# Kernel tuning notes

Hardware: AMD Instinct MI355X
Metric: run time of the kernel (lower is better)

Reference implementation:

```python
import jax, jax.numpy as jnp
import numpy as np

B, T, I, U = 64, 1024, 512, 1024


def ternary_quantize(w):
    # alpha = mean|w|; threshold = 0.7*alpha; map to {-alpha, 0, alpha}
    alpha = jnp.mean(jnp.abs(w))
    thr = 0.7 * alpha
    w_t = jnp.where(jnp.abs(w) < thr, jnp.zeros_like(w), jnp.sign(w))
    return alpha * w_t


def setup_inputs() -> dict:
    key = jax.random.key(0)
    k1, k2, k3 = jax.random.split(key, 3)
    x = jax.random.normal(k1, (B, T, I), dtype=jnp.float32)
    kernel = jax.random.normal(k2, (I, 4 * U), dtype=jnp.float32) * 0.05
    recurrent_kernel = jax.random.normal(k3, (U, 4 * U), dtype=jnp.float32) * 0.05
    # keras unit_forget_bias: zeros except ones on the forget-gate quarter
    bias = jnp.concatenate([jnp.zeros((U,)), jnp.ones((U,)), jnp.zeros((2 * U,))]).astype(jnp.float32)
    return {"x": x, "kernel": kernel, "recurrent_kernel": recurrent_kernel, "bias": bias}


def reference(x, kernel, recurrent_kernel, bias):
    kq = ternary_quantize(kernel)            # [I, 4U]
    rq = ternary_quantize(recurrent_kernel)  # [U, 4U]
    # Precompute input projection for all timesteps (math identical to per-step matmul)
    xz = jnp.einsum('bti,ig->btg', x, kq) + bias  # [B, T, 4U]
    xz_t = jnp.transpose(xz, (1, 0, 2))           # [T, B, 4U]

    def step(carry, zx):
        h, c = carry
        z = zx + h @ rq                            # [B, 4U]
        zi, zf, zg, zo = jnp.split(z, 4, axis=-1)  # keras gate order i, f, c, o
        i = jax.nn.sigmoid(zi)
        f = jax.nn.sigmoid(zf)
        g = jnp.tanh(zg)
        o = jax.nn.sigmoid(zo)
        c_new = f * c + i * g
        h_new = o * jnp.tanh(c_new)
        return (h_new, c_new), h_new

    h0 = jnp.zeros((x.shape[0], U), dtype=x.dtype)
    c0 = jnp.zeros((x.shape[0], U), dtype=x.dtype)
    _, hs = jax.lax.scan(step, (h0, c0), xz_t)     # hs: [T, B, U]
    return jnp.transpose(hs, (1, 0, 2))            # return_sequences=True -> [B, T, U]
```

## Files before the change

### kernel.cpp

```cpp
#include <hip/hip_runtime.h>
#include <hip/hip_bf16.h>


typedef __attribute__((ext_vector_type(8))) __bf16 bf16x8;
typedef __attribute__((ext_vector_type(4))) float f32x4;

#define NWG 256
#define WGT 512
#define T_N 1024

__global__ void absum_kernel(const float* __restrict__ w, int n,
                             double* __restrict__ partial) {
  __shared__ double sd[256];
  double s = 0.0;
  for (int i = blockIdx.x * 256 + threadIdx.x; i < n; i += 256 * 256)
    s += fabs((double)w[i]);
  sd[threadIdx.x] = s;
  __syncthreads();
  for (int k = 128; k > 0; k >>= 1) {
    if (threadIdx.x < k) sd[threadIdx.x] += sd[threadIdx.x + k];
    __syncthreads();
  }
  if (threadIdx.x == 0) partial[blockIdx.x] = sd[0];
}

__global__ void alpha_finalize(const double* __restrict__ pk,
                               const double* __restrict__ pr,
                               float* __restrict__ alphas) {
  __shared__ double sd[256];
  int t = threadIdx.x;
  sd[t] = pk[t];
  __syncthreads();
  for (int s = 128; s > 0; s >>= 1) {
    if (t < s) sd[t] += sd[t + s];
    __syncthreads();
  }
  if (t == 0) alphas[0] = (float)(sd[0] / (512.0 * 4096.0));
  __syncthreads();
  sd[t] = pr[t];
  __syncthreads();
  for (int s = 128; s > 0; s >>= 1) {
    if (t < s) sd[t] += sd[t + s];
    __syncthreads();
  }
  if (t == 0) alphas[1] = (float)(sd[0] / (1024.0 * 4096.0));
}

__global__ void quant_kernel(const float* __restrict__ w, int kbits,
                             const float* __restrict__ alphas, int ai,
                             __hip_bfloat16* __restrict__ wt, int total) {
  int idx = blockIdx.x * 256 + threadIdx.x;
  if (idx >= total) return;
  float thr = 0.7f * alphas[ai];
  int K = 1 << kbits;
  int c = idx >> kbits;
  int k = idx & (K - 1);
  float v = w[k * 4096 + (c & 3) * 1024 + (c >> 2)];
  float q = (fabsf(v) < thr) ? 0.0f : ((v > 0.0f) ? 1.0f : ((v < 0.0f) ? -1.0f : 0.0f));
  wt[idx] = __float2bfloat16(q);
}

__device__ __forceinline__ bf16x8 cvt2(f32x4 a, f32x4 b) {
  bf16x8 r;
  r[0] = (__bf16)a[0]; r[1] = (__bf16)a[1];
  r[2] = (__bf16)a[2]; r[3] = (__bf16)a[3];
  r[4] = (__bf16)b[0]; r[5] = (__bf16)b[1];
  r[6] = (__bf16)b[2]; r[7] = (__bf16)b[3];
  return r;
}
__device__ __forceinline__ void ld_cc16(bf16x8* d, const __hip_bfloat16* p) {
  asm volatile("global_load_dwordx4 %0, %1, off sc0 sc1"
               : "=v"(*d) : "v"(p) : "memory");
}
__device__ __forceinline__ void st_cc2(__hip_bfloat16* p, unsigned bits) {
  asm volatile("global_store_short %0, %1, off sc0 sc1" ::"v"(p), "v"(bits)
               : "memory");
}
__device__ __forceinline__ unsigned bf16b(float f) {
  return (unsigned)__builtin_bit_cast(unsigned short, __float2bfloat16(f));
}
__device__ __forceinline__ float sigm(float z) { return 1.0f / (1.0f + __expf(-z)); }
__device__ __forceinline__ float tanhx(float z) {
  float e = __expf(-2.0f * fabsf(z));
  return __builtin_copysignf((1.0f - e) / (1.0f + e), z);
}
__device__ __forceinline__ void wg_barrier_wait(const int* gctr, int g, int tgt,
                                                int* lflag, int epoch,
                                                int lane, int wave) {
  if (wave == 0) {
    const int* p = gctr + (g * 4 + (lane & 3)) * 32;
    for (;;) {
      int v = (lane < 4) ? __hip_atomic_load(p, __ATOMIC_RELAXED,
                                             __HIP_MEMORY_SCOPE_AGENT)
                         : tgt;
      if (__all(v >= tgt)) break;
      __builtin_amdgcn_s_sleep(1);
    }
    if (lane == 0)
      __hip_atomic_store(lflag, epoch, __ATOMIC_RELEASE,
                         __HIP_MEMORY_SCOPE_WORKGROUP);
  }
  while (__hip_atomic_load(lflag, __ATOMIC_ACQUIRE,
                           __HIP_MEMORY_SCOPE_WORKGROUP) < epoch) {}
}

__global__ void __launch_bounds__(WGT, 2)
lstm_persist(const float* __restrict__ bias4, const float* __restrict__ alphas,
             const float* __restrict__ x,
             const __hip_bfloat16* __restrict__ wtk,
             const __hip_bfloat16* __restrict__ wtr,
             __hip_bfloat16* __restrict__ hbuf,
             float* __restrict__ out,
             int* __restrict__ gctr) {
  extern __shared__ char lds[];
  char* lwr = lds;
  float* lz = (float*)(lds + 131072);
  float* lxz = (float*)(lds + 148480);
  int* lflag = (int*)(lds + 157184);

  const int tid = threadIdx.x;
  const int wg = blockIdx.x;
  const int g = wg >> 6;
  const int u = wg & 63;
  const int rb0 = g << 4;
  const int lane = tid & 63;
  const int wave = tid >> 6;
  const int r16 = lane & 15;
  const int kb8 = (lane >> 4) << 3;

  if (tid == 0) *lflag = 0;

  for (int it = tid; it < 8192; it += WGT) {
    int c = it >> 7, kk = (it & 127) << 3;
    bf16x8 v = *(const bf16x8*)(wtr + (size_t)(u * 64 + c) * 1024 + kk);
    *(bf16x8*)(lwr + (c << 11) + ((kk * 2) ^ ((c & 7) << 4))) = v;
  }

  const float ak = alphas[0];
  const float ar = alphas[1];

  const int rl = (tid >> 4) & 15;
  const int ul = tid & 15;
  float bias_c[4];
#pragma unroll
  for (int gg = 0; gg < 4; ++gg)
    bias_c[gg] = bias4[gg * 1024 + u * 16 + ul];
  float cst = 0.0f;
  __hip_bfloat16* hst = hbuf + ((rb0 + rl) << 10) + u * 16 + ul;
  float* outp = out + ((size_t)(rb0 + rl) << 20) + u * 16 + ul;

  const int ks0 = wave << 8;
  float* lzw = lz + wave * 1088;

  const int cw = wave - 4;

  bf16x8 fr[8];

  auto xproj = [&](int tt, int par) {
    const float* xr = x + ((size_t)(rb0 + r16) << 19) + ((size_t)tt << 9) + kb8;
    const __hip_bfloat16* bp =
        wtk + (size_t)(u * 64 + cw * 16 + r16) * 512 + kb8;
    f32x4 a = {0.f, 0.f, 0.f, 0.f};
#pragma unroll
    for (int kw = 0; kw < 16; ++kw) {
      bf16x8 af = cvt2(*(const f32x4*)(xr + kw * 32),
                       *(const f32x4*)(xr + kw * 32 + 4));
      bf16x8 bf = *(const bf16x8*)(bp + kw * 32);
      a = __builtin_amdgcn_mfma_f32_16x16x32_bf16(af, bf, a, 0, 0, 0);
    }
    float* dst = lxz + par * 1088;
#pragma unroll
    for (int j = 0; j < 4; ++j)
      dst[(((lane >> 4) << 2) + j) * 68 + cw * 16 + r16] = a[j];
  };

  __syncthreads();

  if (wave >= 4) xproj(0, 0);
  __syncthreads();

  int tgt = 16;
  int ep = 1;

  for (int t = 0; t < T_N; ++t) {
    if (wave < 4) {
      f32x4 acc[4];
#pragma unroll
      for (int nt = 0; nt < 4; ++nt) acc[nt] = (f32x4){0.f, 0.f, 0.f, 0.f};
      if (t > 0) {
        const __hip_bfloat16* hrow =
            hbuf + ((t & 1) << 16) + ((rb0 + r16) << 10) + ks0 + kb8;
#pragma unroll
        for (int ks = 0; ks < 8; ++ks) ld_cc16(&fr[ks], hrow + (ks << 5));
        asm volatile("s_waitcnt vmcnt(0)" ::: "memory");
        __builtin_amdgcn_sched_barrier(0);
#pragma unroll
        for (int ks = 0; ks < 8; ++ks) {
          int kbyte = (ks0 + (ks << 5) + kb8) << 1;
#pragma unroll
          for (int nt = 0; nt < 4; ++nt) {
            int c = (nt << 4) + r16;
            bf16x8 b = *(const bf16x8*)(lwr + (c << 11) + (kbyte ^ ((c & 7) << 4)));
            acc[nt] = __builtin_amdgcn_mfma_f32_16x16x32_bf16(fr[ks], b, acc[nt], 0, 0, 0);
          }
        }
      }
#pragma unroll
      for (int nt = 0; nt < 4; ++nt) {
#pragma unroll
        for (int j = 0; j < 4; ++j)
          lzw[(((lane >> 4) << 2) + j) * 68 + (nt << 4) + r16] = acc[nt][j];
      }
    }
    __syncthreads();

    float ho = 0.0f;
    if (wave < 4) {
      f32x4 z0 = *(const f32x4*)(lz + 0 * 1088 + rl * 68 + ul * 4);
      f32x4 z1 = *(const f32x4*)(lz + 1 * 1088 + rl * 68 + ul * 4);
      f32x4 z2 = *(const f32x4*)(lz + 2 * 1088 + rl * 68 + ul * 4);
      f32x4 z3 = *(const f32x4*)(lz + 3 * 1088 + rl * 68 + ul * 4);
      f32x4 z = z0 + z1 + z2 + z3;
      f32x4 xv = *(const f32x4*)(lxz + (t & 1) * 1088 + rl * 68 + ul * 4);
      float zi = ak * xv[0] + bias_c[0] + ar * z[0];
      float zf = ak * xv[1] + bias_c[1] + ar * z[1];
      float zg = ak * xv[2] + bias_c[2] + ar * z[2];
      float zo = ak * xv[3] + bias_c[3] + ar * z[3];
      float ig = sigm(zi), fg = sigm(zf), gg = tanhx(zg), og = sigm(zo);
      float cn = fg * cst + ig * gg;
      cst = cn;
      ho = og * tanhx(cn);
      st_cc2(hst + (((t + 1) & 1) << 16), bf16b(ho));
    }
    __syncthreads();

    if (tid == 0)
      __hip_atomic_fetch_add(gctr + (g * 4 + (u & 3)) * 32, 1, __ATOMIC_RELAXED,
                             __HIP_MEMORY_SCOPE_AGENT);

    if (wave < 4) {
      outp[(size_t)t << 10] = ho;
    } else if (t != T_N - 1) {
      xproj(t + 1, (t + 1) & 1);
    }

    wg_barrier_wait(gctr, g, tgt, lflag, ep, lane, wave);
    tgt += 16;
    ++ep;
  }
}

extern "C" void kernel_launch(void* const* d_in, const int* in_sizes, int n_in,
                              void* d_out, int out_size, void* d_ws, size_t ws_size,
                              hipStream_t stream) {
  const float* x = (const float*)d_in[0];
  const float* wk = (const float*)d_in[1];
  const float* wr = (const float*)d_in[2];
  const float* bs = (const float*)d_in[3];
  float* out = (float*)d_out;
  char* ws = (char*)d_ws;

  float* alphas = (float*)(ws + 0);
  int* gctr = (int*)(ws + 256);
  double* pk = (double*)(ws + 4096);
  double* pr = (double*)(ws + 6144);
  __hip_bfloat16* wtk = (__hip_bfloat16*)(ws + 8192);
  __hip_bfloat16* wtr = (__hip_bfloat16*)(ws + 8192 + (4 << 20));
  __hip_bfloat16* hbuf = (__hip_bfloat16*)(ws + 8192 + (12 << 20));

  absum_kernel<<<256, 256, 0, stream>>>(wk, 512 * 4096, pk);
  absum_kernel<<<256, 256, 0, stream>>>(wr, 1024 * 4096, pr);
  alpha_finalize<<<1, 256, 0, stream>>>(pk, pr, alphas);
  quant_kernel<<<(4096 * 512) / 256, 256, 0, stream>>>(wk, 9, alphas, 0, wtk,
                                                       4096 * 512);
  quant_kernel<<<(4096 * 1024) / 256, 256, 0, stream>>>(wr, 10, alphas, 1, wtr,
                                                        4096 * 1024);
  (void)hipMemsetAsync(gctr, 0, 16 * 128, stream);

  const int smem = 131072 + 17408 + 8704 + 128;
  (void)hipFuncSetAttribute((const void*)lstm_persist,
                            hipFuncAttributeMaxDynamicSharedMemorySize, smem);
  void* args[] = {(void*)&bs,  (void*)&alphas, (void*)&x,   (void*)&wtk,
                  (void*)&wtr, (void*)&hbuf,   (void*)&out, (void*)&gctr};
  (void)hipLaunchCooperativeKernel((void*)lstm_persist, dim3(NWG), dim3(WGT),
                                   args, smem, stream);
}
```

Baseline: 12.18 ms.

## Repartition persistent LSTM: recurrent weights in registers, input weights in LDS, per-WG flags

Each workgroup now covers 8 batch rows by 32 units (128 gate columns) instead of 16 rows by 16 units. The recurrent ternary weights are held in VGPRs across all 8 waves and the input-projection weights are staged in LDS, so all waves do both the recurrent MFMA and the x-projection. The per-group atomic counter barrier is replaced by per-workgroup flag stores that one wave polls. Hidden-state writes are coalesced through LDS into 8-byte stores. This trades heavy register pressure and half-empty MFMA rows (8 of 16 rows padded with zeros) for less LDS weight traffic and cheaper sync. The hipMemsetAsync call also drops its stream argument, so it now goes to the default stream rather than the kernel's stream.

```diff
diff --git a/kernel.cpp b/kernel.cpp
--- a/kernel.cpp
+++ b/kernel.cpp
@@ -4,6 +4,7 @@
 
 typedef __attribute__((ext_vector_type(8))) __bf16 bf16x8;
 typedef __attribute__((ext_vector_type(4))) float f32x4;
+typedef __attribute__((ext_vector_type(2))) unsigned int u32x2;
 
 #define NWG 256
 #define WGT 512
@@ -68,13 +69,23 @@
   r[6] = (__bf16)b[2]; r[7] = (__bf16)b[3];
   return r;
 }
-__device__ __forceinline__ void ld_cc16(bf16x8* d, const __hip_bfloat16* p) {
+__device__ __forceinline__ void ld16cc(bf16x8* d, const __hip_bfloat16* p) {
   asm volatile("global_load_dwordx4 %0, %1, off sc0 sc1"
                : "=v"(*d) : "v"(p) : "memory");
 }
-__device__ __forceinline__ void st_cc2(__hip_bfloat16* p, unsigned bits) {
-  asm volatile("global_store_short %0, %1, off sc0 sc1" ::"v"(p), "v"(bits)
+__device__ __forceinline__ void st8cc(__hip_bfloat16* p, u32x2 v) {
+  asm volatile("global_store_dwordx2 %0, %1, off sc0 sc1" ::"v"(p), "v"(v)
                : "memory");
+}
+__device__ __forceinline__ void stflag(int* p, int v) {
+  asm volatile("global_store_dword %0, %1, off sc0 sc1" ::"v"(p), "v"(v)
+               : "memory");
+}
+__device__ __forceinline__ int ldflag(const int* p) {
+  int v;
+  asm volatile("global_load_dword %0, %1, off sc0 sc1\n\ts_waitcnt vmcnt(0)"
+               : "=v"(v) : "v"(p) : "memory");
+  return v;
 }
 __device__ __forceinline__ unsigned bf16b(float f) {
   return (unsigned)__builtin_bit_cast(unsigned short, __float2bfloat16(f));
@@ -84,24 +95,22 @@
   float e = __expf(-2.0f * fabsf(z));
   return __builtin_copysignf((1.0f - e) / (1.0f + e), z);
 }
-__device__ __forceinline__ void wg_barrier_wait(const int* gctr, int g, int tgt,
-                                                int* lflag, int epoch,
-                                                int lane, int wave) {
-  if (wave == 0) {
-    const int* p = gctr + (g * 4 + (lane & 3)) * 32;
+
+__device__ __forceinline__ void wg_wait(const int* fl, int tgt, int* lflag,
+                                        int lane, int wave) {
+  if (wave == 7) {
+    const int* p = fl + (lane & 31);
     for (;;) {
-      int v = (lane < 4) ? __hip_atomic_load(p, __ATOMIC_RELAXED,
-                                             __HIP_MEMORY_SCOPE_AGENT)
-                         : tgt;
+      int v = ldflag(p);
       if (__all(v >= tgt)) break;
       __builtin_amdgcn_s_sleep(1);
     }
     if (lane == 0)
-      __hip_atomic_store(lflag, epoch, __ATOMIC_RELEASE,
+      __hip_atomic_store(lflag, tgt, __ATOMIC_RELEASE,
                          __HIP_MEMORY_SCOPE_WORKGROUP);
   }
   while (__hip_atomic_load(lflag, __ATOMIC_ACQUIRE,
-                           __HIP_MEMORY_SCOPE_WORKGROUP) < epoch) {}
+                           __HIP_MEMORY_SCOPE_WORKGROUP) < tgt) {}
 }
 
 __global__ void __launch_bounds__(WGT, 2)
@@ -113,115 +122,127 @@
              float* __restrict__ out,
              int* __restrict__ gctr) {
   extern __shared__ char lds[];
-  char* lwr = lds;
+  char* lwtk = lds;
   float* lz = (float*)(lds + 131072);
-  float* lxz = (float*)(lds + 148480);
-  int* lflag = (int*)(lds + 157184);
+  float* lxz = (float*)(lds + 147968);
+  unsigned short* lhs = (unsigned short*)(lds + 156416);
+  int* lmeta = (int*)(lds + 156928);
 
   const int tid = threadIdx.x;
   const int wg = blockIdx.x;
-  const int g = wg >> 6;
-  const int u = wg & 63;
-  const int rb0 = g << 4;
   const int lane = tid & 63;
   const int wave = tid >> 6;
   const int r16 = lane & 15;
   const int kb8 = (lane >> 4) << 3;
 
-  if (tid == 0) *lflag = 0;
+  const int g = wg >> 5;
+  const int u = wg & 31;
+  const int rb0 = g << 3;
+  int* flagsg = gctr + 64 + g * 32;
+
+  if (tid == 0) lmeta[0] = 0;
 
   for (int it = tid; it < 8192; it += WGT) {
-    int c = it >> 7, kk = (it & 127) << 3;
-    bf16x8 v = *(const bf16x8*)(wtr + (size_t)(u * 64 + c) * 1024 + kk);
-    *(bf16x8*)(lwr + (c << 11) + ((kk * 2) ^ ((c & 7) << 4))) = v;
+    int c = it >> 6, kk = (it & 63) << 3;
+    bf16x8 v = *(const bf16x8*)(wtk + (size_t)(u * 128 + c) * 512 + kk);
+    *(bf16x8*)(lwtk + (c << 10) + ((kk << 1) ^ ((c & 7) << 4))) = v;
+  }
+
+  const int ks0 = (wave & 3) << 8;
+  bf16x8 bw[8][4];
+  {
+    const __hip_bfloat16* wb =
+        wtr + (size_t)(u * 128 + ((wave >> 2) << 6) + r16) * 1024 + ks0 + kb8;
+#pragma unroll
+    for (int ks = 0; ks < 8; ++ks)
+#pragma unroll
+      for (int nt = 0; nt < 4; ++nt)
+        bw[ks][nt] = *(const bf16x8*)(wb + (size_t)nt * 16 * 1024 + (ks << 5));
   }
 
   const float ak = alphas[0];
   const float ar = alphas[1];
 
-  const int rl = (tid >> 4) & 15;
-  const int ul = tid & 15;
+  const int rl = tid >> 5;
+  const int ul = tid & 31;
   float bias_c[4];
 #pragma unroll
   for (int gg = 0; gg < 4; ++gg)
-    bias_c[gg] = bias4[gg * 1024 + u * 16 + ul];
+    bias_c[gg] = bias4[gg * 1024 + u * 32 + ul];
   float cst = 0.0f;
-  __hip_bfloat16* hst = hbuf + ((rb0 + rl) << 10) + u * 16 + ul;
-  float* outp = out + ((size_t)(rb0 + rl) << 20) + u * 16 + ul;
-
-  const int ks0 = wave << 8;
-  float* lzw = lz + wave * 1088;
-
-  const int cw = wave - 4;
-
-  bf16x8 fr[8];
+  float* outp = out + ((size_t)(rb0 + rl) << 20) + u * 32 + ul;
 
   auto xproj = [&](int tt, int par) {
-    const float* xr = x + ((size_t)(rb0 + r16) << 19) + ((size_t)tt << 9) + kb8;
-    const __hip_bfloat16* bp =
-        wtk + (size_t)(u * 64 + cw * 16 + r16) * 512 + kb8;
+    const float* xr =
+        x + ((size_t)(rb0 + (r16 & 7)) << 19) + ((size_t)tt << 9) + kb8;
+    const int cloc = (wave << 4) + r16;
+    const char* bbase = lwtk + (cloc << 10);
+    const int bxor = (cloc & 7) << 4;
     f32x4 a = {0.f, 0.f, 0.f, 0.f};
 #pragma unroll
     for (int kw = 0; kw < 16; ++kw) {
       bf16x8 af = cvt2(*(const f32x4*)(xr + kw * 32),
                        *(const f32x4*)(xr + kw * 32 + 4));
-      bf16x8 bf = *(const bf16x8*)(bp + kw * 32);
+      bf16x8 bf = *(const bf16x8*)(bbase + ((((kw << 5) + kb8) << 1) ^ bxor));
       a = __builtin_amdgcn_mfma_f32_16x16x32_bf16(af, bf, a, 0, 0, 0);
     }
-    float* dst = lxz + par * 1088;
-#pragma unroll
-    for (int j = 0; j < 4; ++j)
-      dst[(((lane >> 4) << 2) + j) * 68 + cw * 16 + r16] = a[j];
+    if (lane < 32) {
+      float* dst = lxz + par * 1056 + (wave << 4) + (lane & 15);
+#pragma unroll
+      for (int j = 0; j < 4; ++j)
+        dst[(((lane >> 4) << 2) + j) * 132] = a[j];
+    }
   };
 
   __syncthreads();
-
-  if (wave >= 4) xproj(0, 0);
-  __syncthreads();
-
-  int tgt = 16;
-  int ep = 1;
+  xproj(0, 0);
 
   for (int t = 0; t < T_N; ++t) {
-    if (wave < 4) {
+    {
       f32x4 acc[4];
 #pragma unroll
       for (int nt = 0; nt < 4; ++nt) acc[nt] = (f32x4){0.f, 0.f, 0.f, 0.f};
       if (t > 0) {
-        const __hip_bfloat16* hrow =
-            hbuf + ((t & 1) << 16) + ((rb0 + r16) << 10) + ks0 + kb8;
-#pragma unroll
-        for (int ks = 0; ks < 8; ++ks) ld_cc16(&fr[ks], hrow + (ks << 5));
+        bf16x8 fr[8];
+        if (r16 < 8) {
+          const __hip_bfloat16* hrow =
+              hbuf + ((t & 1) << 16) + (g << 13) + (r16 << 10) + ks0 + kb8;
+#pragma unroll
+          for (int ks = 0; ks < 8; ++ks) ld16cc(&fr[ks], hrow + (ks << 5));
+        } else {
+#pragma unroll
+          for (int ks = 0; ks < 8; ++ks)
+#pragma unroll
+            for (int j = 0; j < 8; ++j) fr[ks][j] = (__bf16)0.0f;
+        }
         asm volatile("s_waitcnt vmcnt(0)" ::: "memory");
         __builtin_amdgcn_sched_barrier(0);
 #pragma unroll
-        for (int ks = 0; ks < 8; ++ks) {
-          int kbyte = (ks0 + (ks << 5) + kb8) << 1;
-#pragma unroll
-          for (int nt = 0; nt < 4; ++nt) {
-            int c = (nt << 4) + r16;
-            bf16x8 b = *(const bf16x8*)(lwr + (c << 11) + (kbyte ^ ((c & 7) << 4)));
-            acc[nt] = __builtin_amdgcn_mfma_f32_16x16x32_bf16(fr[ks], b, acc[nt], 0, 0, 0);
-          }
-        }
+        for (int ks = 0; ks < 8; ++ks)
+#pragma unroll
+          for (int nt = 0; nt < 4; ++nt)
+            acc[nt] = __builtin_amdgcn_mfma_f32_16x16x32_bf16(
+                fr[ks], bw[ks][nt], acc[nt], 0, 0, 0);
       }
-#pragma unroll
-      for (int nt = 0; nt < 4; ++nt) {
-#pragma unroll
-        for (int j = 0; j < 4; ++j)
-          lzw[(((lane >> 4) << 2) + j) * 68 + (nt << 4) + r16] = acc[nt][j];
+      if (lane < 32) {
+        float* dst = lz + (wave & 3) * 1056 + ((wave >> 2) << 6) + (lane & 15);
+#pragma unroll
+        for (int nt = 0; nt < 4; ++nt)
+#pragma unroll
+          for (int j = 0; j < 4; ++j)
+            dst[(((lane >> 4) << 2) + j) * 132 + (nt << 4)] = acc[nt][j];
       }
     }
     __syncthreads();
 
     float ho = 0.0f;
-    if (wave < 4) {
-      f32x4 z0 = *(const f32x4*)(lz + 0 * 1088 + rl * 68 + ul * 4);
-      f32x4 z1 = *(const f32x4*)(lz + 1 * 1088 + rl * 68 + ul * 4);
-      f32x4 z2 = *(const f32x4*)(lz + 2 * 1088 + rl * 68 + ul * 4);
-      f32x4 z3 = *(const f32x4*)(lz + 3 * 1088 + rl * 68 + ul * 4);
+    if (tid < 256) {
+      f32x4 z0 = *(const f32x4*)(lz + 0 * 1056 + rl * 132 + (ul << 2));
+      f32x4 z1 = *(const f32x4*)(lz + 1 * 1056 + rl * 132 + (ul << 2));
+      f32x4 z2 = *(const f32x4*)(lz + 2 * 1056 + rl * 132 + (ul << 2));
+      f32x4 z3 = *(const f32x4*)(lz + 3 * 1056 + rl * 132 + (ul << 2));
       f32x4 z = z0 + z1 + z2 + z3;
-      f32x4 xv = *(const f32x4*)(lxz + (t & 1) * 1088 + rl * 68 + ul * 4);
+      f32x4 xv = *(const f32x4*)(lxz + (t & 1) * 1056 + rl * 132 + (ul << 2));
       float zi = ak * xv[0] + bias_c[0] + ar * z[0];
       float zf = ak * xv[1] + bias_c[1] + ar * z[1];
       float zg = ak * xv[2] + bias_c[2] + ar * z[2];
@@ -230,23 +251,23 @@
       float cn = fg * cst + ig * gg;
       cst = cn;
       ho = og * tanhx(cn);
-      st_cc2(hst + (((t + 1) & 1) << 16), bf16b(ho));
-    }
-    __syncthreads();
-
-    if (tid == 0)
-      __hip_atomic_fetch_add(gctr + (g * 4 + (u & 3)) * 32, 1, __ATOMIC_RELAXED,
-                             __HIP_MEMORY_SCOPE_AGENT);
-
-    if (wave < 4) {
-      outp[(size_t)t << 10] = ho;
-    } else if (t != T_N - 1) {
-      xproj(t + 1, (t + 1) & 1);
-    }
-
-    wg_barrier_wait(gctr, g, tgt, lflag, ep, lane, wave);
-    tgt += 16;
-    ++ep;
+      lhs[tid] = (unsigned short)bf16b(ho);
+    }
+    __syncthreads();
+
+    if (wave == 4) {
+      u32x2 dv = *(const u32x2*)(lhs + (lane << 2));
+      __hip_bfloat16* hb = hbuf + (((t + 1) & 1) << 16) + (g << 13) +
+                           ((lane >> 3) << 10) + u * 32 + ((lane & 7) << 2);
+      st8cc(hb, dv);
+      asm volatile("s_waitcnt vmcnt(0)" ::: "memory");
+      if (lane == 0) stflag(flagsg + u, t + 1);
+    }
+
+    if (tid < 256) outp[(size_t)t << 10] = ho;
+    if (t != T_N - 1) xproj(t + 1, (t + 1) & 1);
+
+    wg_wait(flagsg, t + 1, lmeta, lane, wave);
   }
 }
 
@@ -261,7 +282,7 @@
   char* ws = (char*)d_ws;
 
   float* alphas = (float*)(ws + 0);
-  int* gctr = (int*)(ws + 256);
+  int* sync = (int*)(ws + 256);
   double* pk = (double*)(ws + 4096);
   double* pr = (double*)(ws + 6144);
   __hip_bfloat16* wtk = (__hip_bfloat16*)(ws + 8192);
@@ -275,13 +296,13 @@
                                                        4096 * 512);
   quant_kernel<<<(4096 * 1024) / 256, 256, 0, stream>>>(wr, 10, alphas, 1, wtr,
                                                         4096 * 1024);
-  (void)hipMemsetAsync(gctr, 0, 16 * 128, stream);
-
-  const int smem = 131072 + 17408 + 8704 + 128;
+  (void)hipMemsetAsync(sync, 0, 2048);
+
+  const int smem = 131072 + 16896 + 8448 + 512 + 32;
   (void)hipFuncSetAttribute((const void*)lstm_persist,
                             hipFuncAttributeMaxDynamicSharedMemorySize, smem);
   void* args[] = {(void*)&bs,  (void*)&alphas, (void*)&x,   (void*)&wtk,
-                  (void*)&wtr, (void*)&hbuf,   (void*)&out, (void*)&gctr};
+                  (void*)&wtr, (void*)&hbuf,   (void*)&out, (void*)&sync};
   (void)hipLaunchCooperativeKernel((void*)lstm_persist, dim3(NWG), dim3(WGT),
                                    args, smem, stream);
 }
```

After: 10.80 ms. -11.4%, faster.
